# Kernel tuning notes

Measured on AMD Instinct MI355X. Metric: run time of the kernel, lower is better.

Reference implementation:

```python
import jax, jax.numpy as jnp
import numpy as np

N_NODES = 50000
N_EDGES = 800000
D = 96
N_LAYERS = 3


def setup_inputs() -> dict:
    key = jax.random.key(0)
    ks = jax.random.split(key, 2 + 2 * N_LAYERS)
    inp = {
        "x": jax.random.normal(ks[0], (N_NODES, D), dtype=jnp.float32),
        "edge_index": jax.random.randint(ks[1], (2, N_EDGES), 0, N_NODES, dtype=jnp.int64),
    }
    # Xavier-uniform init for the 2-layer MLPs (fan_in=fan_out=D -> limit=sqrt(6/(2D)))
    limit = float(np.sqrt(6.0 / (2 * D)))
    for l in range(N_LAYERS):
        inp[f"w1_{l}"] = jax.random.uniform(ks[2 + 2 * l], (D, D), jnp.float32, -limit, limit)
        inp[f"b1_{l}"] = jnp.zeros((D,), jnp.float32)
        inp[f"w2_{l}"] = jax.random.uniform(ks[3 + 2 * l], (D, D), jnp.float32, -limit, limit)
        inp[f"b2_{l}"] = jnp.zeros((D,), jnp.float32)
    return inp


def reference(x, edge_index, w1_0, b1_0, w2_0, b2_0, w1_1, b1_1, w2_1, b2_1, w1_2, b1_2, w2_2, b2_2):
    src, dst = edge_index[0], edge_index[1]
    n = x.shape[0]
    layers = [(w1_0, b1_0, w2_0, b2_0), (w1_1, b1_1, w2_1, b2_1), (w1_2, b1_2, w2_2, b2_2)]
    xs = [x]
    h = x
    for (w1, b1, w2, b2) in layers:
        # GIN aggregation: sum over incoming neighbor messages, eps = 0
        aggr = jax.ops.segment_sum(h[src], dst, num_segments=n)  # [N, D]
        h = aggr + h  # (1 + eps) * x + sum_j x_j
        h = jnp.maximum(h @ w1 + b1, 0.0) @ w2 + b2  # Linear-ReLU-Linear
        xs.append(h)
    return jnp.concatenate(xs, axis=-1)  # [N, 4*D] since cat=True
```

## Files before the change

### kernel.cpp

```cpp
#include <hip/hip_runtime.h>
#include <hip/hip_bf16.h>

#define D 96
#define SCANB 512
#define ASTR 104
#define WSTR 104

typedef __attribute__((ext_vector_type(8))) short short8;
typedef __attribute__((ext_vector_type(4))) float f32x4v;

__global__ void k_copyx(const float* __restrict__ x, float* __restrict__ out, int n) {
    int idx = blockIdx.x * blockDim.x + threadIdx.x;
    if (idx >= n * 24) return;
    int r = idx / 24, c = idx - r * 24;
    ((float4*)out)[r * 96 + c] = ((const float4*)x)[r * 24 + c];
}

__global__ void k_prep(const float* __restrict__ w10, const float* __restrict__ w20,
                       const float* __restrict__ w11, const float* __restrict__ w21,
                       const float* __restrict__ w12, const float* __restrict__ w22,
                       __hip_bfloat16* __restrict__ wTg) {
    int idx = blockIdx.x * blockDim.x + threadIdx.x;
    if (idx >= 6 * 9216) return;
    int m = idx / 9216, i = idx - m * 9216;
    int k = i / 96, nn = i - k * 96;
    const float* W;
    switch (m) {
        case 0: W = w10; break; case 1: W = w20; break;
        case 2: W = w11; break; case 3: W = w21; break;
        case 4: W = w12; break; default: W = w22; break;
    }
    wTg[(size_t)m * (96 * WSTR) + nn * WSTR + k] = __float2bfloat16(W[k * 96 + nn]);
}

__global__ void k_hist(const int* __restrict__ dst, int* __restrict__ deg, int E) {
    int e = blockIdx.x * blockDim.x + threadIdx.x;
    if (e < E) atomicAdd(&deg[dst[e]], 1);
}

__global__ __launch_bounds__(SCANB) void k_scan1(const int* __restrict__ deg,
                                                 int* __restrict__ rowstart,
                                                 int* __restrict__ bsum, int n) {
    __shared__ int s[SCANB];
    int idx = threadIdx.x, gid = blockIdx.x * SCANB + idx;
    int v = (gid < n) ? deg[gid] : 0;
    s[idx] = v;
    __syncthreads();
    for (int off = 1; off < SCANB; off <<= 1) {
        int u = (idx >= off) ? s[idx - off] : 0;
        __syncthreads();
        s[idx] += u;
        __syncthreads();
    }
    if (gid < n) rowstart[gid] = s[idx] - v;
    if (idx == SCANB - 1) bsum[blockIdx.x] = s[idx];
}

__global__ void k_scan2(const int* __restrict__ bsum, int* __restrict__ boff, int nb) {
    __shared__ int s[128];
    int idx = threadIdx.x;
    int v = (idx < nb) ? bsum[idx] : 0;
    s[idx] = v;
    __syncthreads();
    for (int off = 1; off < 128; off <<= 1) {
        int u = (idx >= off) ? s[idx - off] : 0;
        __syncthreads();
        s[idx] += u;
        __syncthreads();
    }
    if (idx < nb) boff[idx] = s[idx] - v;
}

__global__ void k_scan3(int* __restrict__ rowstart, int* __restrict__ cursor,
                        const int* __restrict__ boff, int n, int E) {
    int gid = blockIdx.x * blockDim.x + threadIdx.x;
    if (gid < n) {
        int v = rowstart[gid] + boff[gid >> 9];
        rowstart[gid] = v;
        cursor[gid] = v;
    }
    if (gid == 0) rowstart[n] = E;
}

__global__ void k_fill(const int* __restrict__ src, const int* __restrict__ dst,
                       int* __restrict__ cursor, int* __restrict__ ecsr, int E) {
    int e = blockIdx.x * blockDim.x + threadIdx.x;
    if (e < E) {
        int p = atomicAdd(&cursor[dst[e]], 1);
        ecsr[p] = src[e];
    }
}

__global__ __launch_bounds__(256) void k_aggr(const float* __restrict__ h,
                                              const int* __restrict__ rowstart,
                                              const int* __restrict__ ecsr,
                                              __hip_bfloat16* __restrict__ t16, int n) {
    int g = (blockIdx.x * 256 + threadIdx.x) >> 5;
    int lane = threadIdx.x & 31;
    if (g >= n || lane >= 24) return;
    const float4* hp = (const float4*)h;
    float4 a = hp[(size_t)g * 24 + lane];
    int e0 = rowstart[g], e1 = rowstart[g + 1];
    int k = e0;
    for (; k + 4 <= e1; k += 4) {
        int s0 = ecsr[k], s1 = ecsr[k + 1], s2 = ecsr[k + 2], s3 = ecsr[k + 3];
        float4 v0 = hp[(size_t)s0 * 24 + lane];
        float4 v1 = hp[(size_t)s1 * 24 + lane];
        float4 v2 = hp[(size_t)s2 * 24 + lane];
        float4 v3 = hp[(size_t)s3 * 24 + lane];
        a.x += v0.x + v1.x + v2.x + v3.x;
        a.y += v0.y + v1.y + v2.y + v3.y;
        a.z += v0.z + v1.z + v2.z + v3.z;
        a.w += v0.w + v1.w + v2.w + v3.w;
    }
    for (; k < e1; k++) {
        int s = ecsr[k];
        float4 v = hp[(size_t)s * 24 + lane];
        a.x += v.x; a.y += v.y; a.z += v.z; a.w += v.w;
    }
    union { __hip_bfloat16 hh[4]; uint2 u; } p;
    p.hh[0] = __float2bfloat16(a.x); p.hh[1] = __float2bfloat16(a.y);
    p.hh[2] = __float2bfloat16(a.z); p.hh[3] = __float2bfloat16(a.w);
    ((uint2*)t16)[(size_t)g * 24 + lane] = p.u;
}

__global__ __launch_bounds__(256) void k_mlpm(const __hip_bfloat16* __restrict__ t16,
                                              const __hip_bfloat16* __restrict__ w1t,
                                              const float* __restrict__ B1,
                                              const __hip_bfloat16* __restrict__ w2t,
                                              const float* __restrict__ B2,
                                              float* __restrict__ hbuf,
                                              float* __restrict__ out,
                                              int n, int ocol) {
    __shared__ __align__(16) short aT[64 * ASTR];
    __shared__ __align__(16) short wS[96 * WSTR];

    const int tid = threadIdx.x;
    const int row0 = blockIdx.x * 64;
    const int lane = tid & 63;
    const int wv = __builtin_amdgcn_readfirstlane(tid >> 6);
    const int wr0 = wv * 16;
    const int quad = lane >> 4;
    const int r = lane & 15;

    {
        const uint2* tsrc = (const uint2*)t16;
        for (int idx = tid; idx < 64 * 24; idx += 256) {
            int rr = idx / 24, c = idx - rr * 24;
            int gr = row0 + rr; if (gr >= n) gr = n - 1;
            *(uint2*)&aT[rr * ASTR + c * 4] = tsrc[(size_t)gr * 24 + c];
        }
        const uint* wsrc = (const uint*)w1t;
        uint* wdst = (uint*)wS;
        for (int idx = tid; idx < 96 * WSTR / 2; idx += 256) wdst[idx] = wsrc[idx];
    }
    __syncthreads();

    short8 af[3];
    #pragma unroll
    for (int ksi = 0; ksi < 3; ksi++)
        af[ksi] = *(const short8*)&aT[(wr0 + r) * ASTR + ksi * 32 + quad * 8];

    f32x4v c1[6];
    #pragma unroll
    for (int nt = 0; nt < 6; nt++) {
        f32x4v c = {0.f, 0.f, 0.f, 0.f};
        #pragma unroll
        for (int ksi = 0; ksi < 3; ksi++) {
            short8 bfr = *(const short8*)&wS[(nt * 16 + r) * WSTR + ksi * 32 + quad * 8];
            c = __builtin_amdgcn_mfma_f32_16x16x32_bf16(af[ksi], bfr, c, 0, 0, 0);
        }
        c1[nt] = c;
    }
    __syncthreads();

    #pragma unroll
    for (int nt = 0; nt < 6; nt++) {
        float bv = B1[nt * 16 + r];
        #pragma unroll
        for (int i = 0; i < 4; i++) {
            float y = fmaxf(c1[nt][i] + bv, 0.f);
            __hip_bfloat16 hb = __float2bfloat16(y);
            aT[(wr0 + quad * 4 + i) * ASTR + nt * 16 + r] = *(short*)&hb;
        }
    }
    {
        const uint* wsrc = (const uint*)w2t;
        uint* wdst = (uint*)wS;
        for (int idx = tid; idx < 96 * WSTR / 2; idx += 256) wdst[idx] = wsrc[idx];
    }
    __syncthreads();

    short8 af2[3];
    #pragma unroll
    for (int ksi = 0; ksi < 3; ksi++)
        af2[ksi] = *(const short8*)&aT[(wr0 + r) * ASTR + ksi * 32 + quad * 8];

    #pragma unroll
    for (int nt = 0; nt < 6; nt++) {
        f32x4v c = {0.f, 0.f, 0.f, 0.f};
        #pragma unroll
        for (int ksi = 0; ksi < 3; ksi++) {
            short8 bfr = *(const short8*)&wS[(nt * 16 + r) * WSTR + ksi * 32 + quad * 8];
            c = __builtin_amdgcn_mfma_f32_16x16x32_bf16(af2[ksi], bfr, c, 0, 0, 0);
        }
        float bv = B2[nt * 16 + r];
        int col = nt * 16 + r;
        #pragma unroll
        for (int i = 0; i < 4; i++) {
            int gr = row0 + wr0 + quad * 4 + i;
            if (gr < n) {
                float v = c[i] + bv;
                hbuf[(size_t)gr * D + col] = v;
                out[(size_t)gr * 384 + ocol + col] = v;
            }
        }
    }
}


extern "C" void kernel_launch(void* const* d_in, const int* in_sizes, int n_in,
                              void* d_out, int out_size, void* d_ws, size_t ws_size,
                              hipStream_t stream) {
    const float* x = (const float*)d_in[0];
    const int* ei = (const int*)d_in[1];
    const int n = in_sizes[0] / D;
    const int E = in_sizes[1] / 2;
    const int* src = ei;
    const int* dst = ei + E;
    float* out = (float*)d_out;

    char* ws = (char*)d_ws;
    __hip_bfloat16* t16 = (__hip_bfloat16*)ws;
    float* hbuf = (float*)(ws + 9600000);
    __hip_bfloat16* wTg = (__hip_bfloat16*)(ws + 28800000);
    int* deg      = (int*)(ws + 28950016);
    int* rowstart = deg + 50048;
    int* cursor   = rowstart + 50056;
    int* bsum     = cursor + 50048;
    int* boff     = bsum + 128;
    int* ecsr     = boff + 128;

    const int nb_scan = (n + SCANB - 1) / SCANB;

    k_copyx<<<(n * 24 + 255) / 256, 256, 0, stream>>>(x, out, n);

    k_prep<<<(6 * 9216 + 255) / 256, 256, 0, stream>>>(
        (const float*)d_in[2], (const float*)d_in[4],
        (const float*)d_in[6], (const float*)d_in[8],
        (const float*)d_in[10], (const float*)d_in[12], wTg);

    hipMemsetAsync(deg, 0, (size_t)n * sizeof(int), stream);
    k_hist<<<(E + 255) / 256, 256, 0, stream>>>(dst, deg, E);
    k_scan1<<<nb_scan, SCANB, 0, stream>>>(deg, rowstart, bsum, n);
    k_scan2<<<1, 128, 0, stream>>>(bsum, boff, nb_scan);
    k_scan3<<<(n + 255) / 256, 256, 0, stream>>>(rowstart, cursor, boff, n, E);
    k_fill<<<(E + 255) / 256, 256, 0, stream>>>(src, dst, cursor, ecsr, E);

    const int aggr_grid = (n * 32 + 255) / 256;
    const int mlp_grid  = (n + 63) / 64;

    for (int l = 0; l < 3; l++) {
        const float* B1 = (const float*)d_in[3 + 4 * l];
        const float* B2 = (const float*)d_in[5 + 4 * l];
        const __hip_bfloat16* w1t = wTg + (size_t)(2 * l) * (96 * WSTR);
        const __hip_bfloat16* w2t = wTg + (size_t)(2 * l + 1) * (96 * WSTR);
        const float* h = (l == 0) ? x : hbuf;
        k_aggr<<<aggr_grid, 256, 0, stream>>>(h, rowstart, ecsr, t16, n);
        k_mlpm<<<mlp_grid, 256, 0, stream>>>(t16, w1t, B1, w2t, B2, hbuf, out, n, (l + 1) * D);
    }
}
```

Baseline: 369.6 us.

## Gather bf16 node features and build CSR via two-level bucketed sort

```diff
diff --git a/kernel.cpp b/kernel.cpp
--- a/kernel.cpp
+++ b/kernel.cpp
@@ -2,18 +2,29 @@
 #include <hip/hip_bf16.h>
 
 #define D 96
-#define SCANB 512
 #define ASTR 104
 #define WSTR 104
+#define NB 512
+#define NG 8
+#define BPB 98
 
 typedef __attribute__((ext_vector_type(8))) short short8;
 typedef __attribute__((ext_vector_type(4))) float f32x4v;
 
-__global__ void k_copyx(const float* __restrict__ x, float* __restrict__ out, int n) {
+__device__ inline float blo(unsigned u) { return __uint_as_float(u << 16); }
+__device__ inline float bhi(unsigned u) { return __uint_as_float(u & 0xffff0000u); }
+
+__global__ void k_copyx(const float* __restrict__ x, float* __restrict__ out,
+                        __hip_bfloat16* __restrict__ h16, int n) {
     int idx = blockIdx.x * blockDim.x + threadIdx.x;
     if (idx >= n * 24) return;
     int r = idx / 24, c = idx - r * 24;
-    ((float4*)out)[r * 96 + c] = ((const float4*)x)[r * 24 + c];
+    float4 v = ((const float4*)x)[r * 24 + c];
+    ((float4*)out)[r * 96 + c] = v;
+    union { __hip_bfloat16 hh[4]; uint2 u; } p;
+    p.hh[0] = __float2bfloat16(v.x); p.hh[1] = __float2bfloat16(v.y);
+    p.hh[2] = __float2bfloat16(v.z); p.hh[3] = __float2bfloat16(v.w);
+    ((uint2*)h16)[r * 24 + c] = p.u;
 }
 
 __global__ void k_prep(const float* __restrict__ w10, const float* __restrict__ w20,
@@ -33,95 +44,124 @@
     wTg[(size_t)m * (96 * WSTR) + nn * WSTR + k] = __float2bfloat16(W[k * 96 + nn]);
 }
 
-__global__ void k_hist(const int* __restrict__ dst, int* __restrict__ deg, int E) {
-    int e = blockIdx.x * blockDim.x + threadIdx.x;
-    if (e < E) atomicAdd(&deg[dst[e]], 1);
-}
-
-__global__ __launch_bounds__(SCANB) void k_scan1(const int* __restrict__ deg,
-                                                 int* __restrict__ rowstart,
-                                                 int* __restrict__ bsum, int n) {
-    __shared__ int s[SCANB];
-    int idx = threadIdx.x, gid = blockIdx.x * SCANB + idx;
-    int v = (gid < n) ? deg[gid] : 0;
-    s[idx] = v;
-    __syncthreads();
-    for (int off = 1; off < SCANB; off <<= 1) {
-        int u = (idx >= off) ? s[idx - off] : 0;
+__global__ __launch_bounds__(256) void k_bcount(const int* __restrict__ dst,
+                                                int* __restrict__ cnt, int E, int nblk) {
+    __shared__ int h[NB];
+    for (int i = threadIdx.x; i < NB; i += 256) h[i] = 0;
+    __syncthreads();
+    int g = blockIdx.x & (NG - 1);
+    int chunk = (E + nblk - 1) / nblk;
+    int e0 = blockIdx.x * chunk, e1 = min(e0 + chunk, E);
+    for (int e = e0 + threadIdx.x; e < e1; e += 256)
+        atomicAdd(&h[dst[e] / BPB], 1);
+    __syncthreads();
+    for (int i = threadIdx.x; i < NB; i += 256)
+        if (h[i]) atomicAdd(&cnt[i * NG + g], h[i]);
+}
+
+__global__ __launch_bounds__(256) void k_bscan(const int* __restrict__ cnt,
+                                               int* __restrict__ basearr,
+                                               int* __restrict__ cursor) {
+    __shared__ int tot[256];
+    int t = threadIdx.x;
+    int v[16]; int s = 0;
+    #pragma unroll
+    for (int i = 0; i < 16; i++) { v[i] = cnt[t * 16 + i]; s += v[i]; }
+    tot[t] = s;
+    __syncthreads();
+    for (int off = 1; off < 256; off <<= 1) {
+        int u = (t >= off) ? tot[t - off] : 0;
         __syncthreads();
-        s[idx] += u;
+        tot[t] += u;
         __syncthreads();
     }
-    if (gid < n) rowstart[gid] = s[idx] - v;
-    if (idx == SCANB - 1) bsum[blockIdx.x] = s[idx];
-}
-
-__global__ void k_scan2(const int* __restrict__ bsum, int* __restrict__ boff, int nb) {
-    __shared__ int s[128];
-    int idx = threadIdx.x;
-    int v = (idx < nb) ? bsum[idx] : 0;
-    s[idx] = v;
-    __syncthreads();
-    for (int off = 1; off < 128; off <<= 1) {
-        int u = (idx >= off) ? s[idx - off] : 0;
-        __syncthreads();
-        s[idx] += u;
-        __syncthreads();
-    }
-    if (idx < nb) boff[idx] = s[idx] - v;
-}
-
-__global__ void k_scan3(int* __restrict__ rowstart, int* __restrict__ cursor,
-                        const int* __restrict__ boff, int n, int E) {
-    int gid = blockIdx.x * blockDim.x + threadIdx.x;
-    if (gid < n) {
-        int v = rowstart[gid] + boff[gid >> 9];
-        rowstart[gid] = v;
-        cursor[gid] = v;
-    }
-    if (gid == 0) rowstart[n] = E;
-}
-
-__global__ void k_fill(const int* __restrict__ src, const int* __restrict__ dst,
-                       int* __restrict__ cursor, int* __restrict__ ecsr, int E) {
-    int e = blockIdx.x * blockDim.x + threadIdx.x;
-    if (e < E) {
-        int p = atomicAdd(&cursor[dst[e]], 1);
-        ecsr[p] = src[e];
-    }
-}
-
-__global__ __launch_bounds__(256) void k_aggr(const float* __restrict__ h,
+    int base = tot[t] - s;
+    #pragma unroll
+    for (int i = 0; i < 16; i++) {
+        basearr[t * 16 + i] = base; cursor[t * 16 + i] = base; base += v[i];
+    }
+}
+
+__global__ __launch_bounds__(256) void k_bscatter(const int* __restrict__ src,
+                                                  const int* __restrict__ dst,
+                                                  int* __restrict__ cursor,
+                                                  uint2* __restrict__ epair,
+                                                  int E, int nblk) {
+    int g = blockIdx.x & (NG - 1);
+    int chunk = (E + nblk - 1) / nblk;
+    int e0 = blockIdx.x * chunk, e1 = min(e0 + chunk, E);
+    for (int e = e0 + threadIdx.x; e < e1; e += 256) {
+        int d = dst[e];
+        int b = d / BPB;
+        int p = atomicAdd(&cursor[b * NG + g], 1);
+        epair[p] = make_uint2((unsigned)src[e], (unsigned)d);
+    }
+}
+
+__global__ __launch_bounds__(256) void k_bfine(const uint2* __restrict__ epair,
+                                               const int* __restrict__ basearr,
+                                               int* __restrict__ rowstart,
+                                               int* __restrict__ ecsr, int n, int E) {
+    __shared__ int cnt[BPB];
+    __shared__ int cur[BPB];
+    int b = blockIdx.x;
+    int nb0 = b * BPB;
+    if (nb0 >= n) return;
+    int nb1 = min(nb0 + BPB, n);
+    int s0 = basearr[b * NG];
+    int s1 = (b == NB - 1) ? E : basearr[(b + 1) * NG];
+    for (int i = threadIdx.x; i < BPB; i += 256) cnt[i] = 0;
+    __syncthreads();
+    for (int e = s0 + threadIdx.x; e < s1; e += 256)
+        atomicAdd(&cnt[(int)epair[e].y - nb0], 1);
+    __syncthreads();
+    if (threadIdx.x == 0) {
+        int run = s0;
+        for (int i = 0; i < nb1 - nb0; i++) { cur[i] = run; run += cnt[i]; }
+    }
+    __syncthreads();
+    for (int i = threadIdx.x; i < nb1 - nb0; i += 256) rowstart[nb0 + i] = cur[i];
+    if (threadIdx.x == 0 && nb1 == n) rowstart[n] = s1;
+    __syncthreads();
+    for (int e = s0 + threadIdx.x; e < s1; e += 256) {
+        uint2 p = epair[e];
+        int pos = atomicAdd(&cur[(int)p.y - nb0], 1);
+        ecsr[pos] = (int)p.x;
+    }
+}
+
+__global__ __launch_bounds__(256) void k_aggr(const __hip_bfloat16* __restrict__ h16,
                                               const int* __restrict__ rowstart,
                                               const int* __restrict__ ecsr,
                                               __hip_bfloat16* __restrict__ t16, int n) {
     int g = (blockIdx.x * 256 + threadIdx.x) >> 5;
     int lane = threadIdx.x & 31;
     if (g >= n || lane >= 24) return;
-    const float4* hp = (const float4*)h;
-    float4 a = hp[(size_t)g * 24 + lane];
+    const uint2* hp = (const uint2*)h16;
+    uint2 u = hp[(size_t)g * 24 + lane];
+    float ax = blo(u.x), ay = bhi(u.x), az = blo(u.y), aw = bhi(u.y);
     int e0 = rowstart[g], e1 = rowstart[g + 1];
     int k = e0;
     for (; k + 4 <= e1; k += 4) {
         int s0 = ecsr[k], s1 = ecsr[k + 1], s2 = ecsr[k + 2], s3 = ecsr[k + 3];
-        float4 v0 = hp[(size_t)s0 * 24 + lane];
-        float4 v1 = hp[(size_t)s1 * 24 + lane];
-        float4 v2 = hp[(size_t)s2 * 24 + lane];
-        float4 v3 = hp[(size_t)s3 * 24 + lane];
-        a.x += v0.x + v1.x + v2.x + v3.x;
-        a.y += v0.y + v1.y + v2.y + v3.y;
-        a.z += v0.z + v1.z + v2.z + v3.z;
-        a.w += v0.w + v1.w + v2.w + v3.w;
+        uint2 v0 = hp[(size_t)s0 * 24 + lane];
+        uint2 v1 = hp[(size_t)s1 * 24 + lane];
+        uint2 v2 = hp[(size_t)s2 * 24 + lane];
+        uint2 v3 = hp[(size_t)s3 * 24 + lane];
+        ax += blo(v0.x) + blo(v1.x) + blo(v2.x) + blo(v3.x);
+        ay += bhi(v0.x) + bhi(v1.x) + bhi(v2.x) + bhi(v3.x);
+        az += blo(v0.y) + blo(v1.y) + blo(v2.y) + blo(v3.y);
+        aw += bhi(v0.y) + bhi(v1.y) + bhi(v2.y) + bhi(v3.y);
     }
     for (; k < e1; k++) {
         int s = ecsr[k];
-        float4 v = hp[(size_t)s * 24 + lane];
-        a.x += v.x; a.y += v.y; a.z += v.z; a.w += v.w;
-    }
-    union { __hip_bfloat16 hh[4]; uint2 u; } p;
-    p.hh[0] = __float2bfloat16(a.x); p.hh[1] = __float2bfloat16(a.y);
-    p.hh[2] = __float2bfloat16(a.z); p.hh[3] = __float2bfloat16(a.w);
-    ((uint2*)t16)[(size_t)g * 24 + lane] = p.u;
+        uint2 v = hp[(size_t)s * 24 + lane];
+        ax += blo(v.x); ay += bhi(v.x); az += blo(v.y); aw += bhi(v.y);
+    }
+    union { __hip_bfloat16 hh[4]; uint2 uu; } p;
+    p.hh[0] = __float2bfloat16(ax); p.hh[1] = __float2bfloat16(ay);
+    p.hh[2] = __float2bfloat16(az); p.hh[3] = __float2bfloat16(aw);
+    ((uint2*)t16)[(size_t)g * 24 + lane] = p.uu;
 }
 
 __global__ __launch_bounds__(256) void k_mlpm(const __hip_bfloat16* __restrict__ t16,
@@ -129,7 +169,7 @@
                                               const float* __restrict__ B1,
                                               const __hip_bfloat16* __restrict__ w2t,
                                               const float* __restrict__ B2,
-                                              float* __restrict__ hbuf,
+                                              __hip_bfloat16* __restrict__ h16,
                                               float* __restrict__ out,
                                               int n, int ocol) {
     __shared__ __align__(16) short aT[64 * ASTR];
@@ -150,8 +190,8 @@
             int gr = row0 + rr; if (gr >= n) gr = n - 1;
             *(uint2*)&aT[rr * ASTR + c * 4] = tsrc[(size_t)gr * 24 + c];
         }
-        const uint* wsrc = (const uint*)w1t;
-        uint* wdst = (uint*)wS;
+        const unsigned* wsrc = (const unsigned*)w1t;
+        unsigned* wdst = (unsigned*)wS;
         for (int idx = tid; idx < 96 * WSTR / 2; idx += 256) wdst[idx] = wsrc[idx];
     }
     __syncthreads();
@@ -185,8 +225,8 @@
         }
     }
     {
-        const uint* wsrc = (const uint*)w2t;
-        uint* wdst = (uint*)wS;
+        const unsigned* wsrc = (const unsigned*)w2t;
+        unsigned* wdst = (unsigned*)wS;
         for (int idx = tid; idx < 96 * WSTR / 2; idx += 256) wdst[idx] = wsrc[idx];
     }
     __syncthreads();
@@ -211,13 +251,12 @@
             int gr = row0 + wr0 + quad * 4 + i;
             if (gr < n) {
                 float v = c[i] + bv;
-                hbuf[(size_t)gr * D + col] = v;
                 out[(size_t)gr * 384 + ocol + col] = v;
+                h16[(size_t)gr * D + col] = __float2bfloat16(v);
             }
         }
     }
 }
-
 
 extern "C" void kernel_launch(void* const* d_in, const int* in_sizes, int n_in,
                               void* d_out, int out_size, void* d_ws, size_t ws_size,
@@ -231,31 +270,30 @@
     float* out = (float*)d_out;
 
     char* ws = (char*)d_ws;
-    __hip_bfloat16* t16 = (__hip_bfloat16*)ws;
-    float* hbuf = (float*)(ws + 9600000);
-    __hip_bfloat16* wTg = (__hip_bfloat16*)(ws + 28800000);
-    int* deg      = (int*)(ws + 28950016);
-    int* rowstart = deg + 50048;
-    int* cursor   = rowstart + 50056;
-    int* bsum     = cursor + 50048;
-    int* boff     = bsum + 128;
-    int* ecsr     = boff + 128;
-
-    const int nb_scan = (n + SCANB - 1) / SCANB;
-
-    k_copyx<<<(n * 24 + 255) / 256, 256, 0, stream>>>(x, out, n);
+    __hip_bfloat16* t16  = (__hip_bfloat16*)ws;
+    __hip_bfloat16* h16  = (__hip_bfloat16*)(ws + 9600000);
+    __hip_bfloat16* wTg  = (__hip_bfloat16*)(ws + 19200000);
+    int*   cnt      = (int*)(ws + 19380000);
+    int*   basearr  = (int*)(ws + 19400000);
+    int*   cursor   = (int*)(ws + 19420000);
+    int*   rowstart = (int*)(ws + 19440000);
+    uint2* epair    = (uint2*)(ws + 19700000);
+    int*   ecsr     = (int*)(ws + 26100000);
+
+    const int NBLK = 256;
+
+    k_copyx<<<(n * 24 + 255) / 256, 256, 0, stream>>>(x, out, h16, n);
 
     k_prep<<<(6 * 9216 + 255) / 256, 256, 0, stream>>>(
         (const float*)d_in[2], (const float*)d_in[4],
         (const float*)d_in[6], (const float*)d_in[8],
         (const float*)d_in[10], (const float*)d_in[12], wTg);
 
-    hipMemsetAsync(deg, 0, (size_t)n * sizeof(int), stream);
-    k_hist<<<(E + 255) / 256, 256, 0, stream>>>(dst, deg, E);
-    k_scan1<<<nb_scan, SCANB, 0, stream>>>(deg, rowstart, bsum, n);
-    k_scan2<<<1, 128, 0, stream>>>(bsum, boff, nb_scan);
-    k_scan3<<<(n + 255) / 256, 256, 0, stream>>>(rowstart, cursor, boff, n, E);
-    k_fill<<<(E + 255) / 256, 256, 0, stream>>>(src, dst, cursor, ecsr, E);
+    hipMemsetAsync(cnt, 0, NB * NG * sizeof(int), stream);
+    k_bcount<<<NBLK, 256, 0, stream>>>(dst, cnt, E, NBLK);
+    k_bscan<<<1, 256, 0, stream>>>(cnt, basearr, cursor);
+    k_bscatter<<<NBLK, 256, 0, stream>>>(src, dst, cursor, epair, E, NBLK);
+    k_bfine<<<NB, 256, 0, stream>>>(epair, basearr, rowstart, ecsr, n, E);
 
     const int aggr_grid = (n * 32 + 255) / 256;
     const int mlp_grid  = (n + 63) / 64;
@@ -265,8 +303,7 @@
         const float* B2 = (const float*)d_in[5 + 4 * l];
         const __hip_bfloat16* w1t = wTg + (size_t)(2 * l) * (96 * WSTR);
         const __hip_bfloat16* w2t = wTg + (size_t)(2 * l + 1) * (96 * WSTR);
-        const float* h = (l == 0) ? x : hbuf;
-        k_aggr<<<aggr_grid, 256, 0, stream>>>(h, rowstart, ecsr, t16, n);
-        k_mlpm<<<mlp_grid, 256, 0, stream>>>(t16, w1t, B1, w2t, B2, hbuf, out, n, (l + 1) * D);
-    }
-}
+        k_aggr<<<aggr_grid, 256, 0, stream>>>(h16, rowstart, ecsr, t16, n);
+        k_mlpm<<<mlp_grid, 256, 0, stream>>>(t16, w1t, B1, w2t, B2, h16, out, n, (l + 1) * D);
+    }
+}
```

Result: faster. 328.6 us (-11.1%).
